# Performance work log

Measured on AMD Instinct MI355X. Metric: run time of the kernel, lower is better.

Reference implementation:

```python
import jax, jax.numpy as jnp
import numpy as np

N_HEADS = 16


def _rope_tables(T, D, dtype):
    # RotaryEmbedding: inv_freq = 1/10000^(arange(0,D,2)/D); emb = cat(freqs, freqs)
    inv_freq = 1.0 / (10000.0 ** (jnp.arange(0, D, 2, dtype=jnp.float32) / D))
    t = jnp.arange(T, dtype=jnp.float32)
    freqs = jnp.einsum('i,j->ij', t, inv_freq)          # [T, D/2]
    emb = jnp.concatenate([freqs, freqs], axis=-1)       # [T, D]
    return jnp.cos(emb).astype(dtype), jnp.sin(emb).astype(dtype)


def _apply_rope(x, cos, sin):
    # x: [B, H, T, D]; cos/sin: [T, D] broadcast over batch and heads
    D = x.shape[-1]
    x1, x2 = x[..., : D // 2], x[..., D // 2:]
    return x * cos + jnp.concatenate([-x2, x1], axis=-1) * sin


def setup_inputs() -> dict:
    key = jax.random.key(0)
    k1, k2, k3 = jax.random.split(key, 3)
    B, T, C = 2, 2048, 2048
    x = jax.random.normal(k1, (B, T, C), dtype=jnp.float32)
    wqkv = jax.random.normal(k2, (3 * C, C), dtype=jnp.float32) * (C ** -0.5)
    wo = jax.random.normal(k3, (C, C), dtype=jnp.float32) * (C ** -0.5)
    return {"x": x, "wqkv": wqkv, "wo": wo}


def reference(x, wqkv, wo):
    B, T, C = x.shape
    H = N_HEADS
    D = C // H
    # fused QKV projection (Linear, no bias): y = x @ W^T
    qkv = jnp.einsum('btc,fc->btf', x, wqkv)             # [B, T, 3C]
    qkv = qkv.reshape(B, T, 3, H, D).transpose(2, 0, 3, 1, 4)  # [3, B, H, T, D]
    q, k, v = qkv[0], qkv[1], qkv[2]
    cos, sin = _rope_tables(T, D, x.dtype)
    q = _apply_rope(q, cos, sin)
    k = _apply_rope(k, cos, sin)
    # causal scaled dot-product attention
    scale = 1.0 / jnp.sqrt(jnp.asarray(D, dtype=x.dtype))
    scores = jnp.einsum('bhtd,bhsd->bhts', q, k) * scale  # [B, H, T, T]
    causal = jnp.tril(jnp.ones((T, T), dtype=bool))
    scores = jnp.where(causal, scores, jnp.finfo(scores.dtype).min)
    attn = jax.nn.softmax(scores, axis=-1)
    out = jnp.einsum('bhts,bhsd->bhtd', attn, v)          # [B, H, T, D]
    out = out.transpose(0, 2, 1, 3).reshape(B, T, C)
    return jnp.einsum('btc,oc->bto', out, wo)
```

## Files before the change

kernel.cpp:

```cpp
#include <hip/hip_runtime.h>
#include <stdint.h>

typedef unsigned short u16;
typedef __attribute__((ext_vector_type(8))) short bf16x8;
typedef __attribute__((ext_vector_type(8))) unsigned short u16x8;
typedef __attribute__((ext_vector_type(4))) unsigned short u16x4;
typedef __attribute__((ext_vector_type(4))) float f32x4;

#define TSEQ 2048
#define CDIM 2048
#define NHEAD 16
#define HDIM 128
#define NB 2
#define QKVROW (3 * CDIM)

__device__ __forceinline__ u16 f2bf(float f) {
  uint32_t u = __builtin_bit_cast(uint32_t, f);
  u += 0x7fffu + ((u >> 16) & 1u);
  return (u16)(u >> 16);
}
__device__ __forceinline__ float bf2f(u16 h) {
  uint32_t u = ((uint32_t)h) << 16;
  return __builtin_bit_cast(float, u);
}

__device__ __forceinline__ void gload_lds16(const void* g, void* lds) {
  __builtin_amdgcn_global_load_lds(
      (const __attribute__((address_space(1))) uint32_t*)g,
      (__attribute__((address_space(3))) uint32_t*)lds,
      16, 0, 0);
}

__global__ void cast_f32_bf16(const float* __restrict__ in, u16* __restrict__ out, int n4) {
  int i = blockIdx.x * blockDim.x + threadIdx.x;
  if (i >= n4) return;
  float4 v = ((const float4*)in)[i];
  u16x4 o;
  o[0] = f2bf(v.x); o[1] = f2bf(v.y); o[2] = f2bf(v.z); o[3] = f2bf(v.w);
  ((u16x4*)out)[i] = o;
}

__device__ __forceinline__ void store_c(float* p, float v) { *p = v; }
__device__ __forceinline__ void store_c(u16* p, float v) { *p = f2bf(v); }

template <typename OutT>
__global__ __launch_bounds__(256) void gemm_bt(const u16* __restrict__ A,
                                               const u16* __restrict__ B,
                                               OutT* __restrict__ C,
                                               int M, int N, int K) {
  __shared__ u16 As[128 * 32];
  __shared__ u16 Bs[128 * 32];
  const int tid = threadIdx.x;
  const int lane = tid & 63;
  const int w = tid >> 6;
  const int wr = w >> 1, wc = w & 1;
  const int l15 = lane & 15, g = lane >> 4;
  const int m0 = blockIdx.y * 128, n0 = blockIdx.x * 128;

  f32x4 acc[4][4];
#pragma unroll
  for (int m = 0; m < 4; ++m)
#pragma unroll
    for (int n = 0; n < 4; ++n)
#pragma unroll
      for (int r = 0; r < 4; ++r) acc[m][n][r] = 0.f;

  for (int kt = 0; kt < K; kt += 32) {
    __syncthreads();
#pragma unroll
    for (int i = 0; i < 2; ++i) {
      int c = i * 256 + tid;
      int row = c >> 2, kk = (c & 3) * 8;
      gload_lds16(A + (size_t)(m0 + row) * K + kt + kk,
                  As + (size_t)(i * 256 + w * 64) * 8);
      gload_lds16(B + (size_t)(n0 + row) * K + kt + kk,
                  Bs + (size_t)(i * 256 + w * 64) * 8);
    }
    asm volatile("s_waitcnt vmcnt(0)" ::: "memory");
    __syncthreads();

    bf16x8 af[4], bfv[4];
#pragma unroll
    for (int m = 0; m < 4; ++m)
      af[m] = *(const bf16x8*)(As + (wr * 64 + m * 16 + l15) * 32 + g * 8);
#pragma unroll
    for (int n = 0; n < 4; ++n)
      bfv[n] = *(const bf16x8*)(Bs + (wc * 64 + n * 16 + l15) * 32 + g * 8);
#pragma unroll
    for (int m = 0; m < 4; ++m)
#pragma unroll
      for (int n = 0; n < 4; ++n)
        acc[m][n] = __builtin_amdgcn_mfma_f32_16x16x32_bf16(af[m], bfv[n], acc[m][n], 0, 0, 0);
  }

#pragma unroll
  for (int m = 0; m < 4; ++m) {
    int row = m0 + wr * 64 + m * 16 + g * 4;
#pragma unroll
    for (int n = 0; n < 4; ++n) {
      int col = n0 + wc * 64 + n * 16 + l15;
#pragma unroll
      for (int r = 0; r < 4; ++r)
        store_c(C + (size_t)(row + r) * N + col, acc[m][n][r]);
    }
  }
}

__global__ void rope_inplace(u16* __restrict__ qkv) {
  int idx = blockIdx.x * 256 + threadIdx.x;
  int i = idx & 63;
  int h = (idx >> 6) & (NHEAD - 1);
  int t = (idx >> 10) & (TSEQ - 1);
  int b = idx >> 21;
  size_t rowb = (size_t)(b * TSEQ + t) * QKVROW;
  int col = h * HDIM + i;
  float q1 = bf2f(qkv[rowb + col]);
  float q2 = bf2f(qkv[rowb + col + 64]);
  float k1 = bf2f(qkv[rowb + CDIM + col]);
  float k2 = bf2f(qkv[rowb + CDIM + col + 64]);

  float inv = powf(10000.0f, -(float)i * (1.0f / 64.0f));
  float ang = (float)t * inv;
  float sn, cs;
  sincosf(ang, &sn, &cs);

  const float scale = 0.08838834764831845f;
  qkv[rowb + col]              = f2bf((q1 * cs - q2 * sn) * scale);
  qkv[rowb + col + 64]         = f2bf((q2 * cs + q1 * sn) * scale);
  qkv[rowb + CDIM + col]       = f2bf(k1 * cs - k2 * sn);
  qkv[rowb + CDIM + col + 64]  = f2bf(k2 * cs + k1 * sn);
}

__global__ __launch_bounds__(256) void attn(const u16* __restrict__ qkv,
                                            u16* __restrict__ Og) {
  __shared__ u16 Qs[64 * 128];
  __shared__ u16 Ks[64 * 128];
  __shared__ u16 Vt[128 * 64];
  const int tid = threadIdx.x;
  const int lane = tid & 63;
  const int w = tid >> 6;
  const int l15 = lane & 15, g = lane >> 4;
  const int qt = blockIdx.x;
  const int q0 = qt * 64;
  const int bh = blockIdx.y;
  const int b = bh >> 4, h = bh & (NHEAD - 1);
  const u16* Qb = qkv + (size_t)(b * TSEQ) * QKVROW + h * HDIM;
  const u16* Kb = Qb + CDIM;
  const u16* Vb = Qb + 2 * CDIM;

#pragma unroll
  for (int i = 0; i < 4; ++i) {
    int c = i * 256 + tid;
    int row = c >> 4;
    int irb = ((c & 15) * 16) ^ ((row & 7) << 4);
    gload_lds16((const char*)(Qb + (size_t)(q0 + row) * QKVROW) + irb,
                (char*)Qs + (i * 256 + w * 64) * 16);
  }
  asm volatile("s_waitcnt vmcnt(0)" ::: "memory");
  __syncthreads();

  bf16x8 qf[4];
#pragma unroll
  for (int dk = 0; dk < 4; ++dk) {
    int row = w * 16 + l15;
    int byte = row * 256 + dk * 64 + g * 16;
    byte ^= ((row & 7) << 4);
    qf[dk] = *(const bf16x8*)((const char*)Qs + byte);
  }

  float mrow[4], lrow[4];
  f32x4 oacc[8];
#pragma unroll
  for (int r = 0; r < 4; ++r) { mrow[r] = -1e30f; lrow[r] = 0.f; }
#pragma unroll
  for (int f = 0; f < 8; ++f)
#pragma unroll
    for (int r = 0; r < 4; ++r) oacc[f][r] = 0.f;

  u16* Ps = Qs;

  for (int ti = 0; ti <= qt; ++ti) {
    const int k0 = ti * 64;
    __syncthreads();
#pragma unroll
    for (int i = 0; i < 4; ++i) {
      int c = i * 256 + tid;
      int row = c >> 4;
      int irb = ((c & 15) * 16) ^ ((row & 7) << 4);
      gload_lds16((const char*)(Kb + (size_t)(k0 + row) * QKVROW) + irb,
                  (char*)Ks + (i * 256 + w * 64) * 16);
    }
#pragma unroll
    for (int i = 0; i < 4; ++i) {
      int c = i * 256 + tid;
      int kr = c >> 4;
      int d0 = (c & 15) * 8;
      u16x8 v = *(const u16x8*)(Vb + (size_t)(k0 + kr) * QKVROW + d0);
#pragma unroll
      for (int j = 0; j < 8; ++j) {
        int d = d0 + j;
        int byte = d * 128 + kr * 2;
        byte ^= (((d ^ (d >> 3)) & 7) << 4);
        *(u16*)((char*)Vt + byte) = v[j];
      }
    }
    asm volatile("s_waitcnt vmcnt(0)" ::: "memory");
    __syncthreads();

    f32x4 sfr[4];
#pragma unroll
    for (int jf = 0; jf < 4; ++jf)
#pragma unroll
      for (int r = 0; r < 4; ++r) sfr[jf][r] = 0.f;
#pragma unroll
    for (int dk = 0; dk < 4; ++dk) {
#pragma unroll
      for (int jf = 0; jf < 4; ++jf) {
        int row = jf * 16 + l15;
        int byte = row * 256 + dk * 64 + g * 16;
        byte ^= ((row & 7) << 4);
        bf16x8 kf = *(const bf16x8*)((const char*)Ks + byte);
        sfr[jf] = __builtin_amdgcn_mfma_f32_16x16x32_bf16(qf[dk], kf, sfr[jf], 0, 0, 0);
      }
    }
    if (ti == qt) {
#pragma unroll
      for (int jf = 0; jf < 4; ++jf) {
        int colg = jf * 16 + l15;
#pragma unroll
        for (int r = 0; r < 4; ++r) {
          int rowg = w * 16 + g * 4 + r;
          if (colg > rowg) sfr[jf][r] = -1e30f;
        }
      }
    }
    float al[4];
#pragma unroll
    for (int r = 0; r < 4; ++r) {
      float pm = fmaxf(fmaxf(sfr[0][r], sfr[1][r]), fmaxf(sfr[2][r], sfr[3][r]));
      pm = fmaxf(pm, __shfl_xor(pm, 1));
      pm = fmaxf(pm, __shfl_xor(pm, 2));
      pm = fmaxf(pm, __shfl_xor(pm, 4));
      pm = fmaxf(pm, __shfl_xor(pm, 8));
      float mn = fmaxf(mrow[r], pm);
      al[r] = __expf(mrow[r] - mn);
      mrow[r] = mn;
    }
    float psum[4] = {0.f, 0.f, 0.f, 0.f};
#pragma unroll
    for (int jf = 0; jf < 4; ++jf)
#pragma unroll
      for (int r = 0; r < 4; ++r) {
        float p = __expf(sfr[jf][r] - mrow[r]);
        sfr[jf][r] = p;
        psum[r] += p;
      }
#pragma unroll
    for (int r = 0; r < 4; ++r) {
      float s = psum[r];
      s += __shfl_xor(s, 1);
      s += __shfl_xor(s, 2);
      s += __shfl_xor(s, 4);
      s += __shfl_xor(s, 8);
      lrow[r] = lrow[r] * al[r] + s;
#pragma unroll
      for (int f = 0; f < 8; ++f) oacc[f][r] *= al[r];
    }
#pragma unroll
    for (int jf = 0; jf < 4; ++jf)
#pragma unroll
      for (int r = 0; r < 4; ++r) {
        int row = g * 4 + r;
        int byte = w * 2048 + row * 128 + (jf * 16 + l15) * 2;
        byte ^= ((row & 7) << 4);
        *(u16*)((char*)Ps + byte) = f2bf(sfr[jf][r]);
      }
#pragma unroll
    for (int ks = 0; ks < 2; ++ks) {
      int pbyte = w * 2048 + l15 * 128 + ks * 64 + g * 16;
      pbyte ^= ((l15 & 7) << 4);
      bf16x8 pa = *(const bf16x8*)((const char*)Ps + pbyte);
#pragma unroll
      for (int df = 0; df < 8; ++df) {
        int d = df * 16 + l15;
        int vbyte = d * 128 + ks * 64 + g * 16;
        vbyte ^= (((d ^ (d >> 3)) & 7) << 4);
        bf16x8 vf = *(const bf16x8*)((const char*)Vt + vbyte);
        oacc[df] = __builtin_amdgcn_mfma_f32_16x16x32_bf16(pa, vf, oacc[df], 0, 0, 0);
      }
    }
  }

#pragma unroll
  for (int r = 0; r < 4; ++r) {
    float inv = 1.0f / lrow[r];
    int trow = q0 + w * 16 + g * 4 + r;
    size_t base = ((size_t)(b * TSEQ + trow)) * CDIM + h * HDIM;
#pragma unroll
    for (int df = 0; df < 8; ++df)
      Og[base + df * 16 + l15] = f2bf(oacc[df][r] * inv);
  }
}

extern "C" void kernel_launch(void* const* d_in, const int* in_sizes, int n_in,
                              void* d_out, int out_size, void* d_ws, size_t ws_size,
                              hipStream_t stream) {
  const float* x = (const float*)d_in[0];
  const float* wqkv = (const float*)d_in[1];
  const float* wo = (const float*)d_in[2];
  float* out = (float*)d_out;

  const size_t M = (size_t)NB * TSEQ;
  char* ws = (char*)d_ws;
  u16* wqkvb = (u16*)ws;  ws += (size_t)3 * CDIM * CDIM * 2;
  u16* wob   = (u16*)ws;  ws += (size_t)CDIM * CDIM * 2;
  u16* qkvb  = (u16*)ws;  ws += M * QKVROW * 2;
  u16* xb    = (u16*)ws;  ws += M * CDIM * 2;
  u16* Og    = xb;
  const size_t needed = (size_t)(ws - (char*)d_ws);
  if (ws_size < needed) return;

  cast_f32_bf16<<<(M * CDIM / 4 + 255) / 256, 256, 0, stream>>>(x, xb, (int)(M * CDIM / 4));
  cast_f32_bf16<<<(3 * CDIM * CDIM / 4 + 255) / 256, 256, 0, stream>>>(wqkv, wqkvb, 3 * CDIM * CDIM / 4);
  cast_f32_bf16<<<(CDIM * CDIM / 4 + 255) / 256, 256, 0, stream>>>(wo, wob, CDIM * CDIM / 4);

  gemm_bt<u16><<<dim3(3 * CDIM / 128, M / 128), 256, 0, stream>>>(xb, wqkvb, qkvb,
                                                                  (int)M, 3 * CDIM, CDIM);
  rope_inplace<<<(NB * TSEQ * NHEAD * 64) / 256, 256, 0, stream>>>(qkvb);

  attn<<<dim3(TSEQ / 64, NB * NHEAD), 256, 0, stream>>>(qkvb, Og);

  gemm_bt<float><<<dim3(CDIM / 128, M / 128), 256, 0, stream>>>(Og, wob, out,
                                                                (int)M, CDIM, CDIM);
}
```

Baseline: 534.2 us.

## Prefetch next K/V tile into registers, reverse tile order, use DPP reductions

The attention loop now issues global loads for the next K and V tile into registers before computing on the current tile, then writes them to LDS after the PV MFMAs. This overlaps memory latency with compute. The V transpose is regrouped so each thread writes 4-element vectors instead of scalar u16 stores. Blocks are launched in reverse query-tile order so the longest causal rows start first, and the row max/sum shuffles are replaced with DPP moves. The cost is higher register pressure from holding 8 prefetch vectors per thread, and one extra barrier per iteration.

```diff
diff --git a/kernel.cpp b/kernel.cpp
--- a/kernel.cpp
+++ b/kernel.cpp
@@ -29,6 +29,26 @@
       (const __attribute__((address_space(1))) uint32_t*)g,
       (__attribute__((address_space(3))) uint32_t*)lds,
       16, 0, 0);
+}
+
+template <int CTRL>
+__device__ __forceinline__ float dpp_mov(float x) {
+  int t = __builtin_amdgcn_update_dpp(0, __builtin_bit_cast(int, x), CTRL, 0xf, 0xf, true);
+  return __builtin_bit_cast(float, t);
+}
+__device__ __forceinline__ float red_max16(float x) {
+  x = fmaxf(x, dpp_mov<0xB1>(x));
+  x = fmaxf(x, dpp_mov<0x4E>(x));
+  x = fmaxf(x, dpp_mov<0x141>(x));
+  x = fmaxf(x, dpp_mov<0x140>(x));
+  return x;
+}
+__device__ __forceinline__ float red_sum16(float x) {
+  x += dpp_mov<0xB1>(x);
+  x += dpp_mov<0x4E>(x);
+  x += dpp_mov<0x141>(x);
+  x += dpp_mov<0x140>(x);
+  return x;
 }
 
 __global__ void cast_f32_bf16(const float* __restrict__ in, u16* __restrict__ out, int n4) {
@@ -140,7 +160,7 @@
   const int lane = tid & 63;
   const int w = tid >> 6;
   const int l15 = lane & 15, g = lane >> 4;
-  const int qt = blockIdx.x;
+  const int qt = (int)gridDim.x - 1 - (int)blockIdx.x;
   const int q0 = qt * 64;
   const int bh = blockIdx.y;
   const int b = bh >> 4, h = bh & (NHEAD - 1);
@@ -148,6 +168,9 @@
   const u16* Kb = Qb + CDIM;
   const u16* Vb = Qb + 2 * CDIM;
 
+  const int v_kv4 = tid & 15;
+  const int v_d0 = (tid >> 4) * 8;
+
 #pragma unroll
   for (int i = 0; i < 4; ++i) {
     int c = i * 256 + tid;
@@ -156,6 +179,18 @@
     gload_lds16((const char*)(Qb + (size_t)(q0 + row) * QKVROW) + irb,
                 (char*)Qs + (i * 256 + w * 64) * 16);
   }
+  u16x8 kreg[4], vreg[4];
+#pragma unroll
+  for (int i = 0; i < 4; ++i) {
+    int c = i * 256 + tid;
+    int row = c >> 4;
+    int irb = ((c & 15) * 16) ^ ((row & 7) << 4);
+    kreg[i] = *(const u16x8*)((const char*)(Kb + (size_t)row * QKVROW) + irb);
+  }
+#pragma unroll
+  for (int jj = 0; jj < 4; ++jj)
+    vreg[jj] = *(const u16x8*)(Vb + (size_t)(v_kv4 * 4 + jj) * QKVROW + v_d0);
+
   asm volatile("s_waitcnt vmcnt(0)" ::: "memory");
   __syncthreads();
 
@@ -168,6 +203,22 @@
     qf[dk] = *(const bf16x8*)((const char*)Qs + byte);
   }
 
+#pragma unroll
+  for (int i = 0; i < 4; ++i) {
+    int c = i * 256 + tid;
+    *(u16x8*)((char*)Ks + c * 16) = kreg[i];
+  }
+#pragma unroll
+  for (int j = 0; j < 8; ++j) {
+    int d = v_d0 + j;
+    int byte = d * 128 + v_kv4 * 8;
+    byte ^= (((d ^ (d >> 3)) & 7) << 4);
+    u16x4 p;
+    p[0] = vreg[0][j]; p[1] = vreg[1][j]; p[2] = vreg[2][j]; p[3] = vreg[3][j];
+    *(u16x4*)((char*)Vt + byte) = p;
+  }
+  __syncthreads();
+
   float mrow[4], lrow[4];
   f32x4 oacc[8];
 #pragma unroll
@@ -180,32 +231,19 @@
   u16* Ps = Qs;
 
   for (int ti = 0; ti <= qt; ++ti) {
-    const int k0 = ti * 64;
-    __syncthreads();
-#pragma unroll
-    for (int i = 0; i < 4; ++i) {
-      int c = i * 256 + tid;
-      int row = c >> 4;
-      int irb = ((c & 15) * 16) ^ ((row & 7) << 4);
-      gload_lds16((const char*)(Kb + (size_t)(k0 + row) * QKVROW) + irb,
-                  (char*)Ks + (i * 256 + w * 64) * 16);
-    }
-#pragma unroll
-    for (int i = 0; i < 4; ++i) {
-      int c = i * 256 + tid;
-      int kr = c >> 4;
-      int d0 = (c & 15) * 8;
-      u16x8 v = *(const u16x8*)(Vb + (size_t)(k0 + kr) * QKVROW + d0);
-#pragma unroll
-      for (int j = 0; j < 8; ++j) {
-        int d = d0 + j;
-        int byte = d * 128 + kr * 2;
-        byte ^= (((d ^ (d >> 3)) & 7) << 4);
-        *(u16*)((char*)Vt + byte) = v[j];
-      }
-    }
-    asm volatile("s_waitcnt vmcnt(0)" ::: "memory");
-    __syncthreads();
+    if (ti < qt) {
+      const int kn = (ti + 1) * 64;
+#pragma unroll
+      for (int i = 0; i < 4; ++i) {
+        int c = i * 256 + tid;
+        int row = c >> 4;
+        int irb = ((c & 15) * 16) ^ ((row & 7) << 4);
+        kreg[i] = *(const u16x8*)((const char*)(Kb + (size_t)(kn + row) * QKVROW) + irb);
+      }
+#pragma unroll
+      for (int jj = 0; jj < 4; ++jj)
+        vreg[jj] = *(const u16x8*)(Vb + (size_t)(kn + v_kv4 * 4 + jj) * QKVROW + v_d0);
+    }
 
     f32x4 sfr[4];
 #pragma unroll
@@ -238,10 +276,7 @@
 #pragma unroll
     for (int r = 0; r < 4; ++r) {
       float pm = fmaxf(fmaxf(sfr[0][r], sfr[1][r]), fmaxf(sfr[2][r], sfr[3][r]));
-      pm = fmaxf(pm, __shfl_xor(pm, 1));
-      pm = fmaxf(pm, __shfl_xor(pm, 2));
-      pm = fmaxf(pm, __shfl_xor(pm, 4));
-      pm = fmaxf(pm, __shfl_xor(pm, 8));
+      pm = red_max16(pm);
       float mn = fmaxf(mrow[r], pm);
       al[r] = __expf(mrow[r] - mn);
       mrow[r] = mn;
@@ -257,11 +292,7 @@
       }
 #pragma unroll
     for (int r = 0; r < 4; ++r) {
-      float s = psum[r];
-      s += __shfl_xor(s, 1);
-      s += __shfl_xor(s, 2);
-      s += __shfl_xor(s, 4);
-      s += __shfl_xor(s, 8);
+      float s = red_sum16(psum[r]);
       lrow[r] = lrow[r] * al[r] + s;
 #pragma unroll
       for (int f = 0; f < 8; ++f) oacc[f][r] *= al[r];
@@ -289,6 +320,25 @@
         oacc[df] = __builtin_amdgcn_mfma_f32_16x16x32_bf16(pa, vf, oacc[df], 0, 0, 0);
       }
     }
+
+    __syncthreads();
+    if (ti < qt) {
+#pragma unroll
+      for (int i = 0; i < 4; ++i) {
+        int c = i * 256 + tid;
+        *(u16x8*)((char*)Ks + c * 16) = kreg[i];
+      }
+#pragma unroll
+      for (int j = 0; j < 8; ++j) {
+        int d = v_d0 + j;
+        int byte = d * 128 + v_kv4 * 8;
+        byte ^= (((d ^ (d >> 3)) & 7) << 4);
+        u16x4 p;
+        p[0] = vreg[0][j]; p[1] = vreg[1][j]; p[2] = vreg[2][j]; p[3] = vreg[3][j];
+        *(u16x4*)((char*)Vt + byte) = p;
+      }
+    }
+    __syncthreads();
   }
 
 #pragma unroll
```

Measured after the change: 500.3 us. 1.07x faster.
